# Kernel optimization log

Hardware: AMD Instinct MI355X
Metric: run time of the kernel (lower is better)

## Reference

```python
import jax, jax.numpy as jnp
import numpy as np

B, IN, OUT, COND, N, H = 512, 256, 256, 128, 8, 64
DP = max(1, int(OUT * 0.25))          # 64 periodic units (cos+sin -> 2*DP outputs)
DN = OUT - 2 * DP                     # 128 non-periodic units
TPE = IN * DP + IN * DN + DN          # params per expert
TOTAL = N * TPE


def setup_inputs() -> dict:
    key = jax.random.key(0)
    ks = jax.random.split(key, 16)
    s_in = np.sqrt(2.0 / IN).astype(np.float32)
    inp = {
        "x": jax.random.normal(ks[0], (B, IN), jnp.float32),
        "cond": jax.random.normal(ks[1], (B, COND), jnp.float32),
        # expert base weights (torch: randn * sqrt(2/in))
        "base_wp": jax.random.normal(ks[2], (N, IN, DP), jnp.float32) * s_in,
        "base_wn": jax.random.normal(ks[3], (N, IN, DN), jnp.float32) * s_in,
        "base_bn": jnp.zeros((N, DN), jnp.float32),
        # hypernet: Linear(cond,H) -> ReLU -> Linear(H, TOTAL)
        "hW1": jax.random.normal(ks[4], (COND, H), jnp.float32) / np.sqrt(COND),
        "hb1": jnp.zeros((H,), jnp.float32),
        "hW2": jax.random.normal(ks[5], (H, TOTAL), jnp.float32) / np.sqrt(H),
        "hb2": jnp.zeros((TOTAL,), jnp.float32),
        # gating: Linear(cond,3N) -> ReLU -> Linear(3N, N)
        "gW1": jax.random.normal(ks[6], (COND, 3 * N), jnp.float32) / np.sqrt(COND),
        "gb1": jnp.zeros((3 * N,), jnp.float32),
        "gW2": jax.random.normal(ks[7], (3 * N, N), jnp.float32) / np.sqrt(3 * N),
        "gb2": jnp.zeros((N,), jnp.float32),
    }
    return inp


def reference(x, cond, base_wp, base_wn, base_bn,
              hW1, hb1, hW2, hb2, gW1, gb1, gW2, gb2):
    bsz = x.shape[0]
    # hypernet -> per-sample dynamic deltas
    h = jax.nn.relu(cond @ hW1 + hb1)
    delta = (h @ hW2 + hb2).reshape(bsz, N, TPE)
    d_wp = delta[:, :, : IN * DP].reshape(bsz, N, IN, DP)
    d_wn = delta[:, :, IN * DP: IN * DP + IN * DN].reshape(bsz, N, IN, DN)
    d_bn = delta[:, :, IN * DP + IN * DN:]                  # (B, N, DN)

    # periodic branch: per-sample, per-expert mat-vec then cos/sin
    wp = base_wp[None] + d_wp                                # (B,N,IN,DP)
    per = jnp.einsum('bi,bnip->bnp', x, wp)                  # (B,N,DP)
    per_cos, per_sin = jnp.cos(per), jnp.sin(per)

    # non-periodic branch
    wn = base_wn[None] + d_wn                                # (B,N,IN,DN)
    non = jnp.einsum('bi,bnip->bnp', x, wn) + base_bn[None] + d_bn
    non = jax.nn.relu(non)                                   # (B,N,DN)

    # gating over experts
    logits = jax.nn.relu(cond @ gW1 + gb1) @ gW2 + gb2       # (B,N)
    gw = jax.nn.softmax(logits, axis=1)[:, :, None]          # (B,N,1)

    cos_c = jnp.sum(per_cos * gw, axis=1)
    sin_c = jnp.sum(per_sin * gw, axis=1)
    non_c = jnp.sum(non * gw, axis=1)
    return jnp.concatenate([cos_c, sin_c, non_c], axis=-1)   # (B, 2*DP+DN)
```

## Files before the change

kernel.cpp:

```cpp
#include <hip/hip_runtime.h>
#include <math.h>

#define BB     512
#define INF    256
#define CONDF  128
#define NEXP   8
#define HDIM   64
#define TPE    49280
#define TOTC   394240
#define NSPLIT 16
#define CW     1536
#define KB     261

#define AZ_OFF 0u
#define BT_OFF 17104896u
#define P_OFF  68419584u
#define GW_OFF 93585408u
#define CB_OFF 93601792u

typedef __bf16          bf16x8 __attribute__((ext_vector_type(8)));
typedef unsigned short  us8    __attribute__((ext_vector_type(8)));
typedef float           f32x4  __attribute__((ext_vector_type(4)));

__device__ __forceinline__ unsigned short f2bf(float f) {
  unsigned u = __builtin_bit_cast(unsigned, f);
  u += 0x7fffu + ((u >> 16) & 1u);
  return (unsigned short)(u >> 16);
}
__device__ __forceinline__ float bf2f(unsigned short u) {
  return __builtin_bit_cast(float, ((unsigned)u) << 16);
}

__device__ __forceinline__ void gld16(const void* g, const void* l) {
  __builtin_amdgcn_global_load_lds(
      (const __attribute__((address_space(1))) unsigned int*)g,
      (__attribute__((address_space(3))) unsigned int*)l, 16, 0, 0);
}

__global__ void k_bt(const float* __restrict__ hW2, unsigned short* __restrict__ Bt,
                     const float* __restrict__ bwp, const float* __restrict__ bwn,
                     const float* __restrict__ bbn, const float* __restrict__ hb2,
                     float* __restrict__ colbias,
                     const float* __restrict__ x, const float* __restrict__ cond,
                     const float* __restrict__ hW1, const float* __restrict__ hb1,
                     const float* __restrict__ gW1, const float* __restrict__ gb1,
                     const float* __restrict__ gW2, const float* __restrict__ gb2,
                     unsigned short* __restrict__ Az, float* __restrict__ gw) {
  const int bx = blockIdx.x;
  const int tid = threadIdx.x;

  if (bx >= 1536) {
    const int b = bx - 1536;
    __shared__ float xs[INF], cs[CONDF], hs[HDIM], g1[24], ls[8], es[8];
    xs[tid] = x[b * INF + tid];
    if (tid < CONDF) cs[tid] = cond[b * CONDF + tid];
    __syncthreads();
    if (tid < HDIM) {
      float acc = hb1[tid];
      for (int q = 0; q < CONDF; ++q) acc = fmaf(cs[q], hW1[q * HDIM + tid], acc);
      hs[tid] = fmaxf(acc, 0.f);
    }
    if (tid >= 64 && tid < 88) {
      const int r = tid - 64;
      float acc = gb1[r];
      for (int q = 0; q < CONDF; ++q) acc = fmaf(cs[q], gW1[q * 24 + r], acc);
      g1[r] = fmaxf(acc, 0.f);
    }
    __syncthreads();
    if (tid < NEXP) {
      float acc = gb2[tid];
      for (int j = 0; j < 24; ++j) acc = fmaf(g1[j], gW2[j * NEXP + tid], acc);
      ls[tid] = acc;
    }
    __syncthreads();
    if (tid < NEXP) {
      float m = ls[0];
      for (int j = 1; j < NEXP; ++j) m = fmaxf(m, ls[j]);
      es[tid] = expf(ls[tid] - m);
    }
    __syncthreads();
    if (tid < NEXP) {
      float s = 0.f;
      for (int j = 0; j < NEXP; ++j) s += es[j];
      gw[b * NEXP + tid] = es[tid] / s;
    }
    const int t0 = tid >> 5, ig = tid & 31;
#pragma unroll
    for (int tt = 0; tt < 8; ++tt) {
      const int t = tt * 8 + t0;
      const float hv = hs[t];
      us8 o;
#pragma unroll
      for (int j = 0; j < 8; ++j) o[j] = f2bf(hv * xs[ig * 8 + j]);
      *(us8*)(Az + ((size_t)(t * 4 + (ig >> 3)) * BB + b) * 64 + (ig & 7) * 8) = o;
    }
    Az[((size_t)(256 + (tid >> 6)) * BB + b) * 64 + (tid & 63)] = f2bf(xs[tid]);
    if (tid < HDIM) Az[((size_t)260 * BB + b) * 64 + tid] = f2bf(hs[tid]);
    return;
  }

  const int t = bx / 24, rem = bx % 24, ne = rem / 3, sec = rem % 3;
  const size_t base = (size_t)t * TOTC + (size_t)ne * TPE + (sec ? 16384 : 0);
  const int dst  = sec ? 128 : 64;
  const int poff = (sec == 2) ? 64 : 0;
  const int cbase = ne * 192 + (sec == 0 ? 0 : (sec == 1 ? 64 : 128));
  __shared__ __align__(16) unsigned short Ls[64 * 256];
#pragma unroll
  for (int it = 0; it < 16; ++it) {
    const int f = it * 256 + tid;
    const int i = f >> 4, p4 = (f & 15) * 4;
    const int e = i >> 3, q = i & 7;
    f32x4 v = *(const f32x4*)(hW2 + base + (size_t)i * dst + poff + p4);
#pragma unroll
    for (int j = 0; j < 4; ++j) {
      const int p = p4 + j;
      Ls[(p << 8) + (((e ^ (p & 31)) << 3) | q)] = f2bf(v[j]);
    }
  }
  if (tid < 64) {
    const int c2 = bx, ne2 = c2 / 192, r2 = c2 % 192;
#pragma unroll
    for (int kb = 0; kb < 5; ++kb) {
      const int j = kb * 64 + tid;
      float v;
      if (j < 256) {
        const int i = j;
        if (r2 < 64) v = bwp[(ne2 * INF + i) * 64 + r2] + hb2[(size_t)ne2 * TPE + i * 64 + r2];
        else         v = bwn[(ne2 * INF + i) * 128 + (r2 - 64)] + hb2[(size_t)ne2 * TPE + 16384 + i * 128 + (r2 - 64)];
      } else {
        const int t2 = j - 256;
        v = (r2 < 64) ? 0.f : hW2[(size_t)t2 * TOTC + (size_t)ne2 * TPE + 49152 + (r2 - 64)];
      }
      Bt[((size_t)(256 + kb) * CW + c2) * 64 + tid] = f2bf(v);
    }
    if (tid == 0)
      colbias[c2] = (r2 < 64) ? 0.f
                  : bbn[ne2 * 128 + (r2 - 64)] + hb2[(size_t)ne2 * TPE + 49152 + (r2 - 64)];
  }
  __syncthreads();
#pragma unroll
  for (int it2 = 0; it2 < 8; ++it2) {
    const int of = it2 * 256 + tid;
    const int p = of >> 5, seg = of & 31, ib = seg >> 3, k8 = seg & 7;
    us8 o = *(const us8*)(&Ls[(p << 8) + ((seg ^ (p & 31)) << 3)]);
    *(us8*)(Bt + ((size_t)(t * 4 + ib) * CW + cbase + p) * 64 + k8 * 8) = o;
  }
}

__launch_bounds__(256, 3)
__global__ void k_gemm(const unsigned short* __restrict__ Az,
                       const unsigned short* __restrict__ Bt,
                       unsigned short* __restrict__ P) {
  const int bid = blockIdx.x;
  const int g  = (bid >> 5) * 8 + (bid & 7);
  const int mt = (bid >> 3) & 3;
  const int nt = g >> 4;
  const int s  = g & 15;
  const int m0 = mt * 128, n0 = nt * 128;
  const int kb0 = s * 16 + (s < 5 ? s : 5);
  const int kb1 = kb0 + 16 + (s < 5 ? 1 : 0);
  const int tid = threadIdx.x;
  __shared__ __align__(16) unsigned short As[128 * 64];
  __shared__ __align__(16) unsigned short Bs[128 * 64];

  f32x4 acc[4][4];
#pragma unroll
  for (int mi = 0; mi < 4; ++mi)
#pragma unroll
    for (int ni = 0; ni < 4; ++ni) acc[mi][ni] = (f32x4){0.f, 0.f, 0.f, 0.f};

  const int wv = tid >> 6, lane = tid & 63;
  const int wm = wv >> 1, wn = wv & 1;
  const int lrow = lane & 15, quad = lane >> 4;
  const int srow = tid >> 3;
  const int sg0  = tid & 7;

  const unsigned short* ab = Az + ((size_t)kb0 * BB + m0) * 64;
  const unsigned short* bb = Bt + ((size_t)kb0 * CW + n0) * 64;

  for (int kb = kb0; kb < kb1; ++kb) {
#pragma unroll
    for (int it = 0; it < 4; ++it) {
      const int r = it * 32 + srow;
      const int ga = sg0 ^ (r & 7);
      const int ldsoff = __builtin_amdgcn_readfirstlane(it * 4096 + wv * 1024);
      gld16(ab + (size_t)r * 64 + ga * 8, (const char*)As + ldsoff);
      gld16(bb + (size_t)r * 64 + ga * 8, (const char*)Bs + ldsoff);
    }
    __syncthreads();
#pragma unroll
    for (int kh = 0; kh < 2; ++kh) {
      bf16x8 af[4], bfr[4];
#pragma unroll
      for (int mi = 0; mi < 4; ++mi) {
        const int r = wm * 64 + mi * 16 + lrow;
        const int ga = (kh * 4 + quad) ^ (r & 7);
        af[mi] = *(const bf16x8*)(As + r * 64 + ga * 8);
      }
#pragma unroll
      for (int ni = 0; ni < 4; ++ni) {
        const int r = wn * 64 + ni * 16 + lrow;
        const int ga = (kh * 4 + quad) ^ (r & 7);
        bfr[ni] = *(const bf16x8*)(Bs + r * 64 + ga * 8);
      }
#pragma unroll
      for (int mi = 0; mi < 4; ++mi)
#pragma unroll
        for (int ni = 0; ni < 4; ++ni)
          acc[mi][ni] = __builtin_amdgcn_mfma_f32_16x16x32_bf16(af[mi], bfr[ni], acc[mi][ni], 0, 0, 0);
    }
    __syncthreads();
    ab += (size_t)BB * 64;
    bb += (size_t)CW * 64;
  }

#pragma unroll
  for (int mi = 0; mi < 4; ++mi) {
    const int row0 = m0 + wm * 64 + mi * 16 + quad * 4;
#pragma unroll
    for (int ni = 0; ni < 4; ++ni) {
      const int col = n0 + wn * 64 + ni * 16 + lrow;
      unsigned short* pp = P + ((size_t)s * BB + row0) * CW + col;
#pragma unroll
      for (int r = 0; r < 4; ++r) pp[(size_t)r * CW] = f2bf(acc[mi][ni][r]);
    }
  }
}

__global__ void k_epi(const unsigned short* __restrict__ P, const float* __restrict__ gw,
                      const float* __restrict__ colbias, float* __restrict__ out) {
  const int b = blockIdx.x;
  const int r = threadIdx.x;
  __shared__ float gws[NEXP];
  if (r < NEXP) gws[r] = gw[b * NEXP + r];
  __syncthreads();
  float co = 0.f, si = 0.f, nc = 0.f;
  for (int n = 0; n < NEXP; ++n) {
    const int c = n * 192 + r;
    float v = colbias[c];
#pragma unroll
    for (int s2 = 0; s2 < NSPLIT; ++s2) v += bf2f(P[((size_t)s2 * BB + b) * CW + c]);
    const float g = gws[n];
    if (r < 64) { co = fmaf(g, cosf(v), co); si = fmaf(g, sinf(v), si); }
    else        { nc = fmaf(g, fmaxf(v, 0.f), nc); }
  }
  if (r < 64) { out[b * 256 + r] = co; out[b * 256 + 64 + r] = si; }
  else        { out[b * 256 + 128 + (r - 64)] = nc; }
}

extern "C" void kernel_launch(void* const* d_in, const int* in_sizes, int n_in,
                              void* d_out, int out_size, void* d_ws, size_t ws_size,
                              hipStream_t stream) {
  const float* x    = (const float*)d_in[0];
  const float* cond = (const float*)d_in[1];
  const float* bwp  = (const float*)d_in[2];
  const float* bwn  = (const float*)d_in[3];
  const float* bbn  = (const float*)d_in[4];
  const float* hW1  = (const float*)d_in[5];
  const float* hb1  = (const float*)d_in[6];
  const float* hW2  = (const float*)d_in[7];
  const float* hb2  = (const float*)d_in[8];
  const float* gW1  = (const float*)d_in[9];
  const float* gb1  = (const float*)d_in[10];
  const float* gW2  = (const float*)d_in[11];
  const float* gb2  = (const float*)d_in[12];
  float* out = (float*)d_out;
  char* ws = (char*)d_ws;

  unsigned short* Az = (unsigned short*)(ws + AZ_OFF);
  unsigned short* Bt = (unsigned short*)(ws + BT_OFF);
  unsigned short* Pp = (unsigned short*)(ws + P_OFF);
  float* gw      = (float*)(ws + GW_OFF);
  float* colbias = (float*)(ws + CB_OFF);

  hipLaunchKernelGGL(k_bt, dim3(2048), dim3(256), 0, stream,
                     hW2, Bt, bwp, bwn, bbn, hb2, colbias,
                     x, cond, hW1, hb1, gW1, gb1, gW2, gb2, Az, gw);
  hipLaunchKernelGGL(k_gemm, dim3(768), dim3(256), 0, stream, Az, Bt, Pp);
  hipLaunchKernelGGL(k_epi, dim3(BB), dim3(192), 0, stream, Pp, gw, colbias, out);
}
```

Before: 219.4 us.

## Restructure Bt packing kernel with dedicated blocks for base-weight and bias rows

Before, the first 64 threads of each transpose block wrote the tail K-blocks (base weights plus hb2, and the hypernet bias rows) one column at a time with strided, uncoalesced loads. Those rows now get their own blocks: 24 blocks transpose the base-weight sums through LDS like the main tiles, and 8 blocks handle the bias row and colbias. The main transpose now batches its global loads ahead of the LDS writes, packs two bf16 values per 32-bit store, and uses a different XOR swizzle. Occupancy is hinted with launch bounds and the small-path shared arrays now reuse one LDS buffer. In exchange there are more blocks and more register pressure from the batched loads.

Measured after the change: 215.0 us. 1.02x faster.

```diff
diff --git a/kernel.cpp b/kernel.cpp
--- a/kernel.cpp
+++ b/kernel.cpp
@@ -37,21 +37,62 @@
       (__attribute__((address_space(3))) unsigned int*)l, 16, 0, 0);
 }
 
-__global__ void k_bt(const float* __restrict__ hW2, unsigned short* __restrict__ Bt,
-                     const float* __restrict__ bwp, const float* __restrict__ bwn,
-                     const float* __restrict__ bbn, const float* __restrict__ hb2,
-                     float* __restrict__ colbias,
-                     const float* __restrict__ x, const float* __restrict__ cond,
-                     const float* __restrict__ hW1, const float* __restrict__ hb1,
-                     const float* __restrict__ gW1, const float* __restrict__ gb1,
-                     const float* __restrict__ gW2, const float* __restrict__ gb2,
-                     unsigned short* __restrict__ Az, float* __restrict__ gw) {
+__global__ __launch_bounds__(256, 4)
+void k_bt(const float* __restrict__ hW2, unsigned short* __restrict__ Bt,
+          const float* __restrict__ bwp, const float* __restrict__ bwn,
+          const float* __restrict__ bbn, const float* __restrict__ hb2,
+          float* __restrict__ colbias,
+          const float* __restrict__ x, const float* __restrict__ cond,
+          const float* __restrict__ hW1, const float* __restrict__ hb1,
+          const float* __restrict__ gW1, const float* __restrict__ gb1,
+          const float* __restrict__ gW2, const float* __restrict__ gb2,
+          unsigned short* __restrict__ Az, float* __restrict__ gw) {
   const int bx = blockIdx.x;
   const int tid = threadIdx.x;
-
-  if (bx >= 1536) {
+  __shared__ __align__(16) unsigned short Ls[64 * 256];
+
+  if (bx >= 2072) {
+    const int ne = bx - 2072;
+    unsigned short* L2 = Ls;
+#pragma unroll
+    for (int it = 0; it < 8; ++it) {
+      const int f = it * 256 + tid;
+      const int t = f >> 5, c4 = (f & 31) * 4;
+      f32x4 v = *(const f32x4*)(hW2 + (size_t)t * TOTC + (size_t)ne * TPE + 49152 + c4);
+#pragma unroll
+      for (int j = 0; j < 4; ++j) L2[t * 129 + c4 + j] = f2bf(v[j]);
+    }
+    if (tid < 192)
+      colbias[ne * 192 + tid] = (tid < 64) ? 0.f
+        : bbn[ne * 128 + (tid - 64)] + hb2[(size_t)ne * TPE + 49152 + (tid - 64)];
+    __syncthreads();
+    if (tid < 128) {
+      const int c = tid;
+#pragma unroll
+      for (int t8 = 0; t8 < 8; ++t8) {
+        us8 o;
+#pragma unroll
+        for (int j = 0; j < 8; ++j) o[j] = L2[(t8 * 8 + j) * 129 + c];
+        *(us8*)(Bt + ((size_t)260 * CW + ne * 192 + 64 + c) * 64 + t8 * 8) = o;
+      }
+    } else {
+      const int cz = (tid - 128) >> 1, hf = (tid - 128) & 1;
+      us8 z = (us8){0, 0, 0, 0, 0, 0, 0, 0};
+#pragma unroll
+      for (int t8 = 0; t8 < 4; ++t8)
+        *(us8*)(Bt + ((size_t)260 * CW + ne * 192 + cz) * 64 + (hf * 4 + t8) * 8) = z;
+    }
+    return;
+  }
+
+  if (bx >= 1536 && bx < 2048) {
     const int b = bx - 1536;
-    __shared__ float xs[INF], cs[CONDF], hs[HDIM], g1[24], ls[8], es[8];
+    float* xs  = (float*)Ls;
+    float* cs  = xs + INF;
+    float* hs  = cs + CONDF;
+    float* g1  = hs + HDIM;
+    float* lsb = g1 + 24;
+    float* es  = lsb + 8;
     xs[tid] = x[b * INF + tid];
     if (tid < CONDF) cs[tid] = cond[b * CONDF + tid];
     __syncthreads();
@@ -70,13 +111,13 @@
     if (tid < NEXP) {
       float acc = gb2[tid];
       for (int j = 0; j < 24; ++j) acc = fmaf(g1[j], gW2[j * NEXP + tid], acc);
-      ls[tid] = acc;
+      lsb[tid] = acc;
     }
     __syncthreads();
     if (tid < NEXP) {
-      float m = ls[0];
-      for (int j = 1; j < NEXP; ++j) m = fmaxf(m, ls[j]);
-      es[tid] = expf(ls[tid] - m);
+      float m = lsb[0];
+      for (int j = 1; j < NEXP; ++j) m = fmaxf(m, lsb[j]);
+      es[tid] = expf(lsb[tid] - m);
     }
     __syncthreads();
     if (tid < NEXP) {
@@ -99,51 +140,74 @@
     return;
   }
 
-  const int t = bx / 24, rem = bx % 24, ne = rem / 3, sec = rem % 3;
-  const size_t base = (size_t)t * TOTC + (size_t)ne * TPE + (sec ? 16384 : 0);
-  const int dst  = sec ? 128 : 64;
-  const int poff = (sec == 2) ? 64 : 0;
-  const int cbase = ne * 192 + (sec == 0 ? 0 : (sec == 1 ? 64 : 128));
-  __shared__ __align__(16) unsigned short Ls[64 * 256];
-#pragma unroll
-  for (int it = 0; it < 16; ++it) {
-    const int f = it * 256 + tid;
-    const int i = f >> 4, p4 = (f & 15) * 4;
-    const int e = i >> 3, q = i & 7;
-    f32x4 v = *(const f32x4*)(hW2 + base + (size_t)i * dst + poff + p4);
-#pragma unroll
-    for (int j = 0; j < 4; ++j) {
-      const int p = p4 + j;
-      Ls[(p << 8) + (((e ^ (p & 31)) << 3) | q)] = f2bf(v[j]);
-    }
-  }
-  if (tid < 64) {
-    const int c2 = bx, ne2 = c2 / 192, r2 = c2 % 192;
-#pragma unroll
-    for (int kb = 0; kb < 5; ++kb) {
-      const int j = kb * 64 + tid;
-      float v;
-      if (j < 256) {
-        const int i = j;
-        if (r2 < 64) v = bwp[(ne2 * INF + i) * 64 + r2] + hb2[(size_t)ne2 * TPE + i * 64 + r2];
-        else         v = bwn[(ne2 * INF + i) * 128 + (r2 - 64)] + hb2[(size_t)ne2 * TPE + 16384 + i * 128 + (r2 - 64)];
-      } else {
-        const int t2 = j - 256;
-        v = (r2 < 64) ? 0.f : hW2[(size_t)t2 * TOTC + (size_t)ne2 * TPE + 49152 + (r2 - 64)];
-      }
-      Bt[((size_t)(256 + kb) * CW + c2) * 64 + tid] = f2bf(v);
-    }
-    if (tid == 0)
-      colbias[c2] = (r2 < 64) ? 0.f
-                  : bbn[ne2 * 128 + (r2 - 64)] + hb2[(size_t)ne2 * TPE + 49152 + (r2 - 64)];
+  const int pq = tid & 15, rg = tid >> 4, p4 = pq * 4;
+  int kbBase, cbase;
+
+  if (bx < 1536) {
+    const int t = bx / 24, rem = bx % 24, ne = rem / 3, sec = rem % 3;
+    const int dst  = sec ? 128 : 64;
+    const int poff = (sec == 2) ? 64 : 0;
+    kbBase = t * 4;
+    cbase  = ne * 192 + sec * 64;
+    const float* src = hW2 + (size_t)t * TOTC + (size_t)ne * TPE
+                       + (sec ? 16384 : 0) + poff + p4;
+    f32x4 va[8], vb[8];
+#pragma unroll
+    for (int it = 0; it < 8; ++it) {
+      const int i0 = rg * 2 + it * 32;
+      va[it] = *(const f32x4*)(src + (size_t)i0 * dst);
+      vb[it] = *(const f32x4*)(src + (size_t)(i0 + 1) * dst);
+    }
+#pragma unroll
+    for (int it = 0; it < 8; ++it) {
+      const int i0 = rg * 2 + it * 32;
+      const int e = i0 >> 3, q0 = i0 & 7;
+#pragma unroll
+      for (int j = 0; j < 4; ++j) {
+        const int p = p4 + j;
+        const unsigned lo = f2bf(va[it][j]), hi = f2bf(vb[it][j]);
+        *(unsigned*)(&Ls[(p << 8) + (((e ^ (p >> 2)) << 3) | q0)]) = lo | (hi << 16);
+      }
+    }
+  } else {
+    const int u = bx - 2048, ne = u / 3, sec = u % 3;
+    const int dst  = sec ? 128 : 64;
+    const int poff = (sec == 2) ? 64 : 0;
+    kbBase = 256;
+    cbase  = ne * 192 + sec * 64;
+    const float* s1 = sec ? (bwn + (size_t)ne * INF * 128 + poff)
+                          : (bwp + (size_t)ne * INF * 64);
+    const float* s2 = hb2 + (size_t)ne * TPE + (sec ? 16384 : 0) + poff;
+#pragma unroll
+    for (int it = 0; it < 8; ++it) {
+      const int i0 = rg * 2 + it * 32;
+      f32x4 a1 = *(const f32x4*)(s1 + (size_t)i0 * dst + p4);
+      f32x4 a2 = *(const f32x4*)(s2 + (size_t)i0 * dst + p4);
+      f32x4 b1 = *(const f32x4*)(s1 + (size_t)(i0 + 1) * dst + p4);
+      f32x4 b2 = *(const f32x4*)(s2 + (size_t)(i0 + 1) * dst + p4);
+      const int e = i0 >> 3, q0 = i0 & 7;
+#pragma unroll
+      for (int j = 0; j < 4; ++j) {
+        const int p = p4 + j;
+        const unsigned lo = f2bf(a1[j] + a2[j]);
+        const unsigned hi = f2bf(b1[j] + b2[j]);
+        *(unsigned*)(&Ls[(p << 8) + (((e ^ (p >> 2)) << 3) | q0)]) = lo | (hi << 16);
+      }
+    }
   }
   __syncthreads();
+  us8 o[8];
+#pragma unroll
+  for (int it2 = 0; it2 < 8; ++it2) {
+    const int of = it2 * 256 + tid;
+    const int p = of >> 5, seg = of & 31;
+    o[it2] = *(const us8*)(&Ls[(p << 8) + ((seg ^ (p >> 2)) << 3)]);
+  }
 #pragma unroll
   for (int it2 = 0; it2 < 8; ++it2) {
     const int of = it2 * 256 + tid;
     const int p = of >> 5, seg = of & 31, ib = seg >> 3, k8 = seg & 7;
-    us8 o = *(const us8*)(&Ls[(p << 8) + ((seg ^ (p & 31)) << 3)]);
-    *(us8*)(Bt + ((size_t)(t * 4 + ib) * CW + cbase + p) * 64 + k8 * 8) = o;
+    *(us8*)(Bt + ((size_t)(kbBase + ib) * CW + cbase + p) * 64 + k8 * 8) = o[it2];
   }
 }
 
@@ -273,7 +337,7 @@
   float* gw      = (float*)(ws + GW_OFF);
   float* colbias = (float*)(ws + CB_OFF);
 
-  hipLaunchKernelGGL(k_bt, dim3(2048), dim3(256), 0, stream,
+  hipLaunchKernelGGL(k_bt, dim3(2080), dim3(256), 0, stream,
                      hW2, Bt, bwp, bwn, bbn, hb2, colbias,
                      x, cond, hW1, hb1, gW1, gb1, gW2, gb2, Az, gw);
   hipLaunchKernelGGL(k_gemm, dim3(768), dim3(256), 0, stream, Az, Bt, Pp);
```
